# Optimization experiments

Measured on AMD Instinct MI355X. Metric: run time of the kernel, lower is better.

Reference implementation:

```python
import jax, jax.numpy as jnp
import numpy as np
from jax import lax

N, D = 16384, 512
E_SPEC, E_SHARED = 8, 2


def setup_inputs() -> dict:
    key = jax.random.key(0)
    ks = jax.random.split(key, 7)
    return {
        "x": jax.random.normal(ks[0], (N, D), dtype=jnp.float32),
        "spec_router_logits": jax.random.normal(ks[1], (N, E_SPEC), dtype=jnp.float32),
        "shared_router_logits": jax.random.normal(ks[2], (N, E_SHARED), dtype=jnp.float32),
        "spec_W": jax.random.normal(ks[3], (E_SPEC, D, D), dtype=jnp.float32) * 0.02,
        "spec_b": jax.random.normal(ks[4], (E_SPEC, D), dtype=jnp.float32) * 0.02,
        "shared_W": jax.random.normal(ks[5], (E_SHARED, D, D), dtype=jnp.float32) * 0.02,
        "shared_b": jax.random.normal(ks[6], (E_SHARED, D), dtype=jnp.float32) * 0.02,
        "top_k": 2,
    }


def reference(x, spec_router_logits, shared_router_logits, spec_W, spec_b, shared_W, shared_b, top_k):
    n, e_spec = spec_router_logits.shape
    # --- specific experts: top-k routing with renormalized weights ---
    spec_probs = jax.nn.softmax(spec_router_logits, axis=1)          # [N, E_spec]
    topk_w, topk_idx = lax.top_k(spec_probs, top_k)                  # [N, K]
    topk_w = topk_w / (jnp.sum(topk_w, axis=1, keepdims=True) + 1e-6)
    # dense per-token per-expert weight matrix (zero for unselected), matching
    # the original dense mask-accumulate loop
    weights = jnp.zeros((n, e_spec), dtype=spec_probs.dtype)
    weights = weights.at[jnp.arange(n)[:, None], topk_idx].add(topk_w)  # [N, E_spec]
    # dense eval of all specific experts (Linear d->d), then weighted combine
    spec_outs = jnp.einsum('nd,edf->enf', x, spec_W) + spec_b[:, None, :]  # [E,N,D]
    spec_out = jnp.einsum('ne,enf->nf', weights, spec_outs)                # [N,D]
    # --- shared experts: soft combine over softmax probs ---
    shared_probs = jax.nn.softmax(shared_router_logits, axis=1)           # [N, E_shared]
    shared_outs = jnp.einsum('nd,edf->enf', x, shared_W) + shared_b[:, None, :]
    shared_out = jnp.einsum('ne,enf->nf', shared_probs, shared_outs)
    return spec_out + shared_out
```

## Files before the change

kernel.cpp:

```cpp
#include <hip/hip_runtime.h>
#include <stdint.h>

typedef unsigned short ushort_t;
typedef __attribute__((ext_vector_type(8))) short short8;
typedef __attribute__((ext_vector_type(4))) float f32x4;
typedef __attribute__((ext_vector_type(4))) unsigned int u32x4;

#define TOK  16384
#define DIM  512
#define NPAIR 64
#define MAXTILES 156

__device__ __forceinline__ unsigned short f2bf(float f) {
  union { float f; uint32_t u; } v; v.f = f;
  uint32_t u = v.u;
  uint32_t r = (u + 0x7fffu + ((u >> 16) & 1u)) >> 16;
  return (unsigned short)r;
}

__global__ void k_router(const float* __restrict__ sl, const float* __restrict__ shl,
                         float* __restrict__ w4, int* __restrict__ pairid,
                         int* __restrict__ cnt) {
  __shared__ int h[NPAIR];
  int tid = threadIdx.x;
  int n = blockIdx.x * 256 + tid;
  if (tid < NPAIR) h[tid] = 0;
  __syncthreads();
  float l[8];
  float m = -1e30f;
#pragma unroll
  for (int i = 0; i < 8; ++i) { l[i] = sl[n*8 + i]; m = fmaxf(m, l[i]); }
  float s = 0.f;
#pragma unroll
  for (int i = 0; i < 8; ++i) { l[i] = expf(l[i] - m); s += l[i]; }
  float inv = 1.f / s;
#pragma unroll
  for (int i = 0; i < 8; ++i) l[i] *= inv;
  int i1 = 0; float v1 = l[0];
#pragma unroll
  for (int i = 1; i < 8; ++i) if (l[i] > v1) { v1 = l[i]; i1 = i; }
  int i2 = -1; float v2 = -1.f;
#pragma unroll
  for (int i = 0; i < 8; ++i) if (i != i1 && l[i] > v2) { v2 = l[i]; i2 = i; }
  float rs = 1.f / (v1 + v2 + 1e-6f);
  float w1 = v1 * rs, w2 = v2 * rs;
  int pmin, pmax; float wa, wb;
  if (i1 < i2) { pmin = i1; pmax = i2; wa = w1; wb = w2; }
  else         { pmin = i2; pmax = i1; wa = w2; wb = w1; }
  float s0 = shl[n*2], s1 = shl[n*2 + 1];
  float mm = fmaxf(s0, s1);
  float e0 = expf(s0 - mm), e1 = expf(s1 - mm);
  float si = 1.f / (e0 + e1);
  w4[n*4 + 0] = wa;
  w4[n*4 + 1] = wb;
  w4[n*4 + 2] = e0 * si;
  w4[n*4 + 3] = e1 * si;
  int p = pmin * 8 + pmax;
  pairid[n] = p;
  atomicAdd(&h[p], 1);
  __syncthreads();
  if (tid < NPAIR && h[tid]) atomicAdd(&cnt[tid], h[tid]);
}

__global__ void k_scan(const int* __restrict__ cnt, int* __restrict__ off,
                       int* __restrict__ cursor, int* __restrict__ tsinfo,
                       int* __restrict__ tileinfo, ushort_t* __restrict__ idx) {
  int l = threadIdx.x;
  int c = cnt[l];
  int t = (c + 127) >> 7;
  int sc = c, st = t;
#pragma unroll
  for (int d = 1; d < 64; d <<= 1) {
    int vc = __shfl_up(sc, d, 64);
    int vt = __shfl_up(st, d, 64);
    if (l >= d) { sc += vc; st += vt; }
  }
  int offv = sc - c, tsv = st - t;
  off[l] = offv; cursor[l] = offv;
  if (l == 63) tsinfo[64] = st;
  for (int q = 0; q < t; ++q) tileinfo[tsv + q] = (l << 16) | q;
  for (int i = l; i < 128; i += 64) idx[TOK + i] = 0;
}

__global__ void k_fill(const int* __restrict__ pairid, int* __restrict__ cursor,
                       ushort_t* __restrict__ idx) {
  __shared__ int hcnt[NPAIR];
  __shared__ int hbase[NPAIR];
  int tid = threadIdx.x;
  int n = blockIdx.x * 256 + tid;
  if (tid < NPAIR) hcnt[tid] = 0;
  __syncthreads();
  int p = pairid[n];
  int r = atomicAdd(&hcnt[p], 1);
  __syncthreads();
  if (tid < NPAIR && hcnt[tid]) hbase[tid] = atomicAdd(&cursor[tid], hcnt[tid]);
  __syncthreads();
  idx[hbase[p] + r] = (ushort_t)n;
}

__global__ void k_gather(const float* __restrict__ x, const ushort_t* __restrict__ idx,
                         ushort_t* __restrict__ xg) {
  int row = blockIdx.x * 4 + (threadIdx.x >> 6);
  int lane = threadIdx.x & 63;
  int t = (int)idx[row];
  const float* src = x + (size_t)t * DIM + lane * 8;
  f32x4 v0 = *(const f32x4*)src;
  f32x4 v1 = *(const f32x4*)(src + 4);
  u32x4 o;
  o[0] = (uint32_t)f2bf(v0[0]) | ((uint32_t)f2bf(v0[1]) << 16);
  o[1] = (uint32_t)f2bf(v0[2]) | ((uint32_t)f2bf(v0[3]) << 16);
  o[2] = (uint32_t)f2bf(v1[0]) | ((uint32_t)f2bf(v1[1]) << 16);
  o[3] = (uint32_t)f2bf(v1[2]) | ((uint32_t)f2bf(v1[3]) << 16);
  *(u32x4*)(xg + (size_t)row * DIM + lane * 8) = o;
}

__global__ void k_trw(const float* __restrict__ wspec, const float* __restrict__ wsh,
                      ushort_t* __restrict__ wt) {
  __shared__ float t[32][33];
  int e = blockIdx.z;
  const float* src = (e < 8) ? (wspec + e * DIM * DIM) : (wsh + (e - 8) * DIM * DIM);
  int tx = threadIdx.x, ty = threadIdx.y;
  int d = blockIdx.y * 32 + ty, f = blockIdx.x * 32 + tx;
  t[ty][tx] = src[d * DIM + f];
  __syncthreads();
  int fo = blockIdx.x * 32 + ty, dd = blockIdx.y * 32 + tx;
  wt[(size_t)e * DIM * DIM + fo * DIM + dd] = f2bf(t[tx][ty]);
}

__global__ __launch_bounds__(256, 3)
void k_moe(const ushort_t* __restrict__ xg, const ushort_t* __restrict__ wt,
           const float* __restrict__ w4, const ushort_t* __restrict__ idx,
           const int* __restrict__ off, const int* __restrict__ cnt,
           const int* __restrict__ tsinfo, const int* __restrict__ tileinfo,
           const float* __restrict__ bspec, const float* __restrict__ bsh,
           float* __restrict__ out) {
  __shared__ ushort_t aB[8192];
  __shared__ ushort_t bB[8192];
  __shared__ float wLT[4 * 128];
  __shared__ float wRT[4 * 128];
  __shared__ float bL[4 * 128];

  const int tid  = threadIdx.x;
  const int lane = tid & 63;
  const int w    = tid >> 6;
  const int wr   = w >> 1, wc = w & 1;

  int bx   = blockIdx.x;
  int slot = (bx & 7) * 78 + (bx >> 3);
  int r    = slot >> 2, cdx = slot & 3;
  if (r >= tsinfo[64]) return;
  int info = tileinfo[r];
  int p = info >> 16, tstart = info & 0xffff;
  const int base = off[p] + (tstart << 7);
  int cl = cnt[p] - (tstart << 7); if (cl > 128) cl = 128;
  const int e0 = p >> 3, e1 = p & 7;
  const int tcol = cdx << 7;

  int soff[4];
#pragma unroll
  for (int q = 0; q < 4; ++q) {
    int pp  = (q << 12) + tid * 16;
    int row = pp >> 7;
    int kb  = (pp & 127) ^ ((row & 7) << 4);
    soff[q] = row * DIM + (kb >> 1);
  }
  const ushort_t* aSrc = xg + (size_t)base * DIM;
  const ushort_t* bSrc = wt + (size_t)tcol * DIM;

  for (int i = tid; i < 512; i += 256) {
    int j = i >> 7, rs = i & 127;
    float wa = 1.f, wb = 1.f;
    if (rs < cl) {
      int t = (int)idx[base + rs];
      wa = w4[t * 4 + j];
      wb = w4[t * 4 + ((j + 1) & 3)];
    }
    wLT[i] = wa;
    wRT[i] = wa / wb;
  }
  for (int i = tid; i < 512; i += 256) {
    int j = i >> 7, col = i & 127;
    int e = (j == 0) ? e0 : (j == 1) ? e1 : (j == 2) ? 8 : 9;
    bL[i] = (e < 8) ? bspec[e * DIM + tcol + col] : bsh[(e - 8) * DIM + tcol + col];
  }

  int aRd[4][2], bRd[4][2];
#pragma unroll
  for (int i = 0; i < 4; ++i) {
    int row = wr * 64 + i * 16 + (lane & 15);
#pragma unroll
    for (int ksl = 0; ksl < 2; ++ksl) {
      int kb = ((ksl << 6) + ((lane >> 4) << 4)) ^ ((row & 7) << 4);
      aRd[i][ksl] = row * 128 + kb;
    }
    int col = wc * 64 + i * 16 + (lane & 15);
#pragma unroll
    for (int ksl = 0; ksl < 2; ++ksl) {
      int kb = ((ksl << 6) + ((lane >> 4) << 4)) ^ ((col & 7) << 4);
      bRd[i][ksl] = col * 128 + kb;
    }
  }

  f32x4 acc[4][4];
#pragma unroll
  for (int a = 0; a < 4; ++a)
#pragma unroll
    for (int b = 0; b < 4; ++b) acc[a][b] = (f32x4){0.f, 0.f, 0.f, 0.f};

#pragma unroll 1
  for (int s = 0; s < 32; ++s) {
    int ks = s >> 2, j = s & 3;
    if (j == 0) {
#pragma unroll
      for (int q = 0; q < 4; ++q)
        __builtin_amdgcn_global_load_lds(
            (const __attribute__((address_space(1))) void*)(aSrc + (ks << 6) + soff[q]),
            (__attribute__((address_space(3))) void*)((char*)aB + (q << 12) + tid * 16),
            16, 0, 0);
    }
    {
      int e = (j == 0) ? e0 : (j == 1) ? e1 : (j == 2) ? 8 : 9;
      const ushort_t* b = bSrc + ((size_t)e << 18) + (ks << 6);
#pragma unroll
      for (int q = 0; q < 4; ++q)
        __builtin_amdgcn_global_load_lds(
            (const __attribute__((address_space(1))) void*)(b + soff[q]),
            (__attribute__((address_space(3))) void*)((char*)bB + (q << 12) + tid * 16),
            16, 0, 0);
    }
    __syncthreads();

    u32x4 af[4][2], bf[4][2];
#pragma unroll
    for (int i = 0; i < 4; ++i)
#pragma unroll
      for (int ksl = 0; ksl < 2; ++ksl) {
        af[i][ksl] = *(const u32x4*)((const char*)aB + aRd[i][ksl]);
        bf[i][ksl] = *(const u32x4*)((const char*)bB + bRd[i][ksl]);
      }
#pragma unroll
    for (int ksl = 0; ksl < 2; ++ksl)
#pragma unroll
      for (int rb = 0; rb < 4; ++rb) {
        short8 a8 = __builtin_bit_cast(short8, af[rb][ksl]);
#pragma unroll
        for (int cb = 0; cb < 4; ++cb) {
          short8 b8 = __builtin_bit_cast(short8, bf[cb][ksl]);
          acc[rb][cb] = __builtin_amdgcn_mfma_f32_16x16x32_bf16(a8, b8, acc[rb][cb], 0, 0, 0);
        }
      }

    if (s < 31) {
#pragma unroll
      for (int rb = 0; rb < 4; ++rb) {
        int rl = wr * 64 + rb * 16 + ((lane >> 4) << 2);
        f32x4 rv = *(const f32x4*)&wRT[(j << 7) + rl];
#pragma unroll
        for (int cb = 0; cb < 4; ++cb) acc[rb][cb] *= rv;
      }
    }
    __syncthreads();
  }

#pragma unroll
  for (int rb = 0; rb < 4; ++rb) {
    int rl = wr * 64 + rb * 16 + ((lane >> 4) << 2);
    f32x4 wv[4];
#pragma unroll
    for (int j = 0; j < 4; ++j) wv[j] = *(const f32x4*)&wLT[(j << 7) + rl];
    int tok[4]; bool pr[4];
#pragma unroll
    for (int q = 0; q < 4; ++q) {
      int rs = rl + q; pr[q] = rs < cl;
      tok[q] = pr[q] ? (int)idx[base + rs] : 0;
    }
#pragma unroll
    for (int cb = 0; cb < 4; ++cb) {
      int cloc = wc * 64 + cb * 16 + (lane & 15);
      f32x4 v = acc[rb][cb] * wv[3];
#pragma unroll
      for (int j = 0; j < 4; ++j) v += wv[j] * bL[(j << 7) + cloc];
#pragma unroll
      for (int q = 0; q < 4; ++q)
        if (pr[q]) out[(size_t)tok[q] * DIM + tcol + cloc] = v[q];
    }
  }
}

extern "C" void kernel_launch(void* const* d_in, const int* in_sizes, int n_in,
                              void* d_out, int out_size, void* d_ws, size_t ws_size,
                              hipStream_t stream) {
  (void)in_sizes; (void)n_in; (void)out_size; (void)ws_size;
  const float* x   = (const float*)d_in[0];
  const float* srl = (const float*)d_in[1];
  const float* shl = (const float*)d_in[2];
  const float* sW  = (const float*)d_in[3];
  const float* sb  = (const float*)d_in[4];
  const float* hW  = (const float*)d_in[5];
  const float* hb  = (const float*)d_in[6];
  float* out = (float*)d_out;

  char* ws = (char*)d_ws;
  float*    w4     = (float*)ws;     ws += TOK * 4 * 4;
  int*      pairid = (int*)ws;       ws += TOK * 4;
  ushort_t* idx    = (ushort_t*)ws;  ws += (TOK + 128) * 2 + 256;
  int*      cntp   = (int*)ws;       ws += NPAIR * 4;
  int*      offp   = (int*)ws;       ws += NPAIR * 4;
  int*      curp   = (int*)ws;       ws += NPAIR * 4;
  int*      tsp    = (int*)ws;       ws += (NPAIR + 1) * 4;
  int*      tinfo  = (int*)ws;       ws += MAXTILES * 4 + 208;
  ushort_t* xg     = (ushort_t*)ws;  ws += (size_t)(TOK + 128) * DIM * 2;
  ushort_t* wt     = (ushort_t*)ws;

  hipMemsetAsync(cntp, 0, NPAIR * sizeof(int), stream);
  k_router<<<TOK / 256, 256, 0, stream>>>(srl, shl, w4, pairid, cntp);
  k_scan<<<1, 64, 0, stream>>>(cntp, offp, curp, tsp, tinfo, idx);
  k_fill<<<TOK / 256, 256, 0, stream>>>(pairid, curp, idx);
  k_gather<<<(TOK + 128) / 4, 256, 0, stream>>>(x, idx, xg);
  dim3 tb(32, 32, 1), tg(16, 16, 10);
  k_trw<<<tg, tb, 0, stream>>>(sW, hW, wt);
  k_moe<<<MAXTILES * 4, 256, 0, stream>>>(xg, wt, w4, idx, offp, cntp, tsp, tinfo,
                                          sb, hb, out);
}
```

Baseline: 91.17 us.

## Merge router into weight-transpose kernel and halve MoE GEMM column tile

```diff
diff --git a/kernel.cpp b/kernel.cpp
--- a/kernel.cpp
+++ b/kernel.cpp
@@ -18,12 +18,28 @@
   return (unsigned short)r;
 }
 
-__global__ void k_router(const float* __restrict__ sl, const float* __restrict__ shl,
-                         float* __restrict__ w4, int* __restrict__ pairid,
-                         int* __restrict__ cnt) {
+__global__ void k_prep(const float* __restrict__ wspec, const float* __restrict__ wsh,
+                       ushort_t* __restrict__ wt,
+                       const float* __restrict__ sl, const float* __restrict__ shl,
+                       float* __restrict__ w4, int* __restrict__ pairid,
+                       int* __restrict__ cnt) {
+  if (blockIdx.z < 10) {
+    __shared__ float t[32][33];
+    int e = blockIdx.z;
+    const float* src = (e < 8) ? (wspec + e * DIM * DIM) : (wsh + (e - 8) * DIM * DIM);
+    int tx = threadIdx.x, ty = threadIdx.y;
+    int d = blockIdx.y * 32 + ty, f = blockIdx.x * 32 + tx;
+    t[ty][tx] = src[d * DIM + f];
+    __syncthreads();
+    int fo = blockIdx.x * 32 + ty, dd = blockIdx.y * 32 + tx;
+    wt[(size_t)e * DIM * DIM + fo * DIM + dd] = f2bf(t[tx][ty]);
+    return;
+  }
+  int blk = blockIdx.y * 16 + blockIdx.x;
+  if (blk >= 16) return;
   __shared__ int h[NPAIR];
-  int tid = threadIdx.x;
-  int n = blockIdx.x * 256 + tid;
+  int tid = threadIdx.y * 32 + threadIdx.x;
+  int n = blk * 1024 + tid;
   if (tid < NPAIR) h[tid] = 0;
   __syncthreads();
   float l[8];
@@ -114,20 +130,7 @@
   *(u32x4*)(xg + (size_t)row * DIM + lane * 8) = o;
 }
 
-__global__ void k_trw(const float* __restrict__ wspec, const float* __restrict__ wsh,
-                      ushort_t* __restrict__ wt) {
-  __shared__ float t[32][33];
-  int e = blockIdx.z;
-  const float* src = (e < 8) ? (wspec + e * DIM * DIM) : (wsh + (e - 8) * DIM * DIM);
-  int tx = threadIdx.x, ty = threadIdx.y;
-  int d = blockIdx.y * 32 + ty, f = blockIdx.x * 32 + tx;
-  t[ty][tx] = src[d * DIM + f];
-  __syncthreads();
-  int fo = blockIdx.x * 32 + ty, dd = blockIdx.y * 32 + tx;
-  wt[(size_t)e * DIM * DIM + fo * DIM + dd] = f2bf(t[tx][ty]);
-}
-
-__global__ __launch_bounds__(256, 3)
+__global__ __launch_bounds__(256, 5)
 void k_moe(const ushort_t* __restrict__ xg, const ushort_t* __restrict__ wt,
            const float* __restrict__ w4, const ushort_t* __restrict__ idx,
            const int* __restrict__ off, const int* __restrict__ cnt,
@@ -135,34 +138,34 @@
            const float* __restrict__ bspec, const float* __restrict__ bsh,
            float* __restrict__ out) {
   __shared__ ushort_t aB[8192];
-  __shared__ ushort_t bB[8192];
+  __shared__ ushort_t bB[4096];
   __shared__ float wLT[4 * 128];
   __shared__ float wRT[4 * 128];
-  __shared__ float bL[4 * 128];
+  __shared__ float bL[4 * 64];
 
   const int tid  = threadIdx.x;
   const int lane = tid & 63;
   const int w    = tid >> 6;
   const int wr   = w >> 1, wc = w & 1;
 
-  int bx   = blockIdx.x;
-  int slot = (bx & 7) * 78 + (bx >> 3);
-  int r    = slot >> 2, cdx = slot & 3;
+  int bx  = blockIdx.x;
+  int r   = bx >> 3, cdx = bx & 7;
   if (r >= tsinfo[64]) return;
   int info = tileinfo[r];
   int p = info >> 16, tstart = info & 0xffff;
   const int base = off[p] + (tstart << 7);
   int cl = cnt[p] - (tstart << 7); if (cl > 128) cl = 128;
   const int e0 = p >> 3, e1 = p & 7;
-  const int tcol = cdx << 7;
-
-  int soff[4];
+  const int tcol = cdx << 6;
+
+  int soffA[4], soffB[2];
 #pragma unroll
   for (int q = 0; q < 4; ++q) {
     int pp  = (q << 12) + tid * 16;
     int row = pp >> 7;
     int kb  = (pp & 127) ^ ((row & 7) << 4);
-    soff[q] = row * DIM + (kb >> 1);
+    soffA[q] = row * DIM + (kb >> 1);
+    if (q < 2) soffB[q] = soffA[q];
   }
   const ushort_t* aSrc = xg + (size_t)base * DIM;
   const ushort_t* bSrc = wt + (size_t)tcol * DIM;
@@ -178,13 +181,13 @@
     wLT[i] = wa;
     wRT[i] = wa / wb;
   }
-  for (int i = tid; i < 512; i += 256) {
-    int j = i >> 7, col = i & 127;
+  if (tid < 256) {
+    int j = tid >> 6, col = tid & 63;
     int e = (j == 0) ? e0 : (j == 1) ? e1 : (j == 2) ? 8 : 9;
-    bL[i] = (e < 8) ? bspec[e * DIM + tcol + col] : bsh[(e - 8) * DIM + tcol + col];
-  }
-
-  int aRd[4][2], bRd[4][2];
+    bL[tid] = (e < 8) ? bspec[e * DIM + tcol + col] : bsh[(e - 8) * DIM + tcol + col];
+  }
+
+  int aRd[4][2], bRd[2][2];
 #pragma unroll
   for (int i = 0; i < 4; ++i) {
     int row = wr * 64 + i * 16 + (lane & 15);
@@ -193,7 +196,10 @@
       int kb = ((ksl << 6) + ((lane >> 4) << 4)) ^ ((row & 7) << 4);
       aRd[i][ksl] = row * 128 + kb;
     }
-    int col = wc * 64 + i * 16 + (lane & 15);
+  }
+#pragma unroll
+  for (int i = 0; i < 2; ++i) {
+    int col = wc * 32 + i * 16 + (lane & 15);
 #pragma unroll
     for (int ksl = 0; ksl < 2; ++ksl) {
       int kb = ((ksl << 6) + ((lane >> 4) << 4)) ^ ((col & 7) << 4);
@@ -201,11 +207,11 @@
     }
   }
 
-  f32x4 acc[4][4];
+  f32x4 acc[4][2];
 #pragma unroll
   for (int a = 0; a < 4; ++a)
 #pragma unroll
-    for (int b = 0; b < 4; ++b) acc[a][b] = (f32x4){0.f, 0.f, 0.f, 0.f};
+    for (int b = 0; b < 2; ++b) acc[a][b] = (f32x4){0.f, 0.f, 0.f, 0.f};
 
 #pragma unroll 1
   for (int s = 0; s < 32; ++s) {
@@ -214,7 +220,7 @@
 #pragma unroll
       for (int q = 0; q < 4; ++q)
         __builtin_amdgcn_global_load_lds(
-            (const __attribute__((address_space(1))) void*)(aSrc + (ks << 6) + soff[q]),
+            (const __attribute__((address_space(1))) void*)(aSrc + (ks << 6) + soffA[q]),
             (__attribute__((address_space(3))) void*)((char*)aB + (q << 12) + tid * 16),
             16, 0, 0);
     }
@@ -222,33 +228,31 @@
       int e = (j == 0) ? e0 : (j == 1) ? e1 : (j == 2) ? 8 : 9;
       const ushort_t* b = bSrc + ((size_t)e << 18) + (ks << 6);
 #pragma unroll
-      for (int q = 0; q < 4; ++q)
+      for (int q = 0; q < 2; ++q)
         __builtin_amdgcn_global_load_lds(
-            (const __attribute__((address_space(1))) void*)(b + soff[q]),
+            (const __attribute__((address_space(1))) void*)(b + soffB[q]),
             (__attribute__((address_space(3))) void*)((char*)bB + (q << 12) + tid * 16),
             16, 0, 0);
     }
     __syncthreads();
 
-    u32x4 af[4][2], bf[4][2];
-#pragma unroll
-    for (int i = 0; i < 4; ++i)
-#pragma unroll
-      for (int ksl = 0; ksl < 2; ++ksl) {
-        af[i][ksl] = *(const u32x4*)((const char*)aB + aRd[i][ksl]);
-        bf[i][ksl] = *(const u32x4*)((const char*)bB + bRd[i][ksl]);
-      }
-#pragma unroll
-    for (int ksl = 0; ksl < 2; ++ksl)
+#pragma unroll
+    for (int ksl = 0; ksl < 2; ++ksl) {
+      u32x4 af[4], bf[2];
+#pragma unroll
+      for (int i = 0; i < 4; ++i) af[i] = *(const u32x4*)((const char*)aB + aRd[i][ksl]);
+#pragma unroll
+      for (int i = 0; i < 2; ++i) bf[i] = *(const u32x4*)((const char*)bB + bRd[i][ksl]);
 #pragma unroll
       for (int rb = 0; rb < 4; ++rb) {
-        short8 a8 = __builtin_bit_cast(short8, af[rb][ksl]);
-#pragma unroll
-        for (int cb = 0; cb < 4; ++cb) {
-          short8 b8 = __builtin_bit_cast(short8, bf[cb][ksl]);
+        short8 a8 = __builtin_bit_cast(short8, af[rb]);
+#pragma unroll
+        for (int cb = 0; cb < 2; ++cb) {
+          short8 b8 = __builtin_bit_cast(short8, bf[cb]);
           acc[rb][cb] = __builtin_amdgcn_mfma_f32_16x16x32_bf16(a8, b8, acc[rb][cb], 0, 0, 0);
         }
       }
+    }
 
     if (s < 31) {
 #pragma unroll
@@ -256,7 +260,7 @@
         int rl = wr * 64 + rb * 16 + ((lane >> 4) << 2);
         f32x4 rv = *(const f32x4*)&wRT[(j << 7) + rl];
 #pragma unroll
-        for (int cb = 0; cb < 4; ++cb) acc[rb][cb] *= rv;
+        for (int cb = 0; cb < 2; ++cb) acc[rb][cb] *= rv;
       }
     }
     __syncthreads();
@@ -275,11 +279,11 @@
       tok[q] = pr[q] ? (int)idx[base + rs] : 0;
     }
 #pragma unroll
-    for (int cb = 0; cb < 4; ++cb) {
-      int cloc = wc * 64 + cb * 16 + (lane & 15);
+    for (int cb = 0; cb < 2; ++cb) {
+      int cloc = wc * 32 + cb * 16 + (lane & 15);
       f32x4 v = acc[rb][cb] * wv[3];
 #pragma unroll
-      for (int j = 0; j < 4; ++j) v += wv[j] * bL[(j << 7) + cloc];
+      for (int j = 0; j < 4; ++j) v += wv[j] * bL[(j << 6) + cloc];
 #pragma unroll
       for (int q = 0; q < 4; ++q)
         if (pr[q]) out[(size_t)tok[q] * DIM + tcol + cloc] = v[q];
@@ -313,12 +317,11 @@
   ushort_t* wt     = (ushort_t*)ws;
 
   hipMemsetAsync(cntp, 0, NPAIR * sizeof(int), stream);
-  k_router<<<TOK / 256, 256, 0, stream>>>(srl, shl, w4, pairid, cntp);
+  dim3 tb(32, 32, 1), tg(16, 16, 11);
+  k_prep<<<tg, tb, 0, stream>>>(sW, hW, wt, srl, shl, w4, pairid, cntp);
   k_scan<<<1, 64, 0, stream>>>(cntp, offp, curp, tsp, tinfo, idx);
   k_fill<<<TOK / 256, 256, 0, stream>>>(pairid, curp, idx);
   k_gather<<<(TOK + 128) / 4, 256, 0, stream>>>(x, idx, xg);
-  dim3 tb(32, 32, 1), tg(16, 16, 10);
-  k_trw<<<tg, tb, 0, stream>>>(sW, hW, wt);
-  k_moe<<<MAXTILES * 4, 256, 0, stream>>>(xg, wt, w4, idx, offp, cntp, tsp, tinfo,
+  k_moe<<<MAXTILES * 8, 256, 0, stream>>>(xg, wt, w4, idx, offp, cntp, tsp, tinfo,
                                           sb, hb, out);
 }
```

Measured after the change: 92.31 us. About the same (+1.3%).
